# Performance work log

Measured on AMD Instinct MI355X. Metric: run time of the kernel, lower is better.

Reference implementation:

```python
import jax, jax.numpy as jnp
import numpy as np

# ---- DMP constants (from DMPParameters with N=5, tau=1, dt=1/(T*l), Dof=9, a_z=25) ----
N_BASIS = 5
T_STEPS = 10
L_SUB = 10
DIM = 9                      # len(state_index)
TAU = 1.0
DT = TAU / (T_STEPS * L_SUB)            # 0.01
TIME_STEPS = int(round(TAU / DT)) + 1   # 101
A_X = 1.0
A_Z = 25.0
B_Z = A_Z / 4.0
_c_np = np.exp(-A_X * np.linspace(0.0, 1.0, N_BASIS))
C = jnp.asarray(_c_np, dtype=jnp.float32)                          # rbf centers
H = jnp.asarray(N_BASIS ** 1.5 / _c_np / A_X, dtype=jnp.float32)   # rbf widths (sigma2)


def _integrate(w, y0, dy0, goal):
    """Euler integration of the DMP dynamical system.
    w: (R, N) basis weights; y0, dy0, goal: (R,) with R = batch*DIM.
    Returns Y: (R, TIME_STEPS) positions."""
    scale = goal - y0  # fixed forcing-term scaling

    def step(carry, _):
        y, z, x = carry
        x = x + (-A_X * x / TAU) * DT                  # canonical system
        psi = jnp.exp(-H * (x - C) ** 2)               # (N,) gaussian rbf
        fx = (w @ psi) * x * scale / jnp.sum(psi)      # (R,) forcing term
        dz = (A_Z * (B_Z * (goal - y) - z) + fx) / TAU
        dy = z / TAU
        y = y + dy * DT
        z = z + dz * DT
        return (y, z, x), y

    z0 = dy0 * TAU
    _, ys = jax.lax.scan(step, (y0, z0, jnp.float32(1.0)), None, length=TIME_STEPS - 1)
    # prepend initial position, transpose to (R, TIME_STEPS)
    return jnp.concatenate([y0[None, :], ys], axis=0).T


def setup_inputs():
    key = jax.random.key(0)
    ks = jax.random.split(key, 4)
    B, D_IN, HID = 16384, 128, 2048
    out_size = DIM * (N_BASIS + 1)  # 54 = N*dim + dim
    return {
        "input": jax.random.normal(ks[0], (B, D_IN), jnp.float32),
        "W0": jax.random.normal(ks[1], (HID, D_IN), jnp.float32) / np.sqrt(D_IN),
        "b0": jnp.full((HID,), 0.1, jnp.float32),
        "W1": jax.random.normal(ks[2], (HID, HID), jnp.float32) / np.sqrt(HID),
        "b1": jnp.full((HID,), 0.1, jnp.float32),
        "Wl": jax.random.normal(ks[3], (out_size, HID), jnp.float32) / np.sqrt(HID),
        "bl": jnp.zeros((out_size,), jnp.float32),
    }


def reference(input, W0, b0, W1, b1, Wl, bl):
    B = input.shape[0]
    # MLP backbone with tanh hidden activation
    h = jnp.tanh(input @ W0.T + b0)
    h = jnp.tanh(h @ W1.T + b1)
    out = (h @ Wl.T + bl) * 100.0                          # (B, DIM*(N+1))
    # split DMP parameters: goal then basis weights
    goal = out[:, :DIM].reshape(-1)                        # (B*DIM,)
    w = out[:, DIM:DIM * (N_BASIS + 1)].reshape(-1, N_BASIS)  # (B*DIM, N)
    y0 = input[:, 7:16].reshape(-1)                        # state_index
    dy0 = input[:, 22:31].reshape(-1)                      # vel_index
    Y = _integrate(w, y0, dy0, goal)                       # (B*DIM, 101)
    y = Y.reshape(B, DIM, TIME_STEPS)[:, :, ::L_SUB]       # (B, DIM, T+1)
    return y[:, :, 1:] - y[:, :, :-1]                      # (B, DIM, T)
```

## Files before the change

kernel.cpp:

```cpp
#include <hip/hip_runtime.h>
#include <hip/hip_fp16.h>
#include <math.h>

typedef _Float16 f16;
typedef _Float16 f16x8 __attribute__((ext_vector_type(8)));
typedef _Float16 f16x4v __attribute__((ext_vector_type(4)));
typedef float f32x4 __attribute__((ext_vector_type(4)));

#define B_SZ 16384
#define D_INP 128
#define HID 2048
#define DIMS 9
#define OUTC 54
#define OUTP 64
#define NZ3 4

__device__ __forceinline__ void load_lds16(const f16* g, f16* l) {
    __builtin_amdgcn_global_load_lds(
        (__attribute__((address_space(1))) void*)(g),
        (__attribute__((address_space(3))) void*)(l),
        16, 0, 0);
}

__device__ __forceinline__ float fast_tanh(float x) {
    float e = __builtin_amdgcn_exp2f(2.885390081777927f * x);
    return 1.0f - 2.0f * __builtin_amdgcn_rcpf(e + 1.0f);
}

#define N4_INP (B_SZ * D_INP / 4)
#define N4_W0  (HID * D_INP / 4)
#define N4_W1  (HID * HID / 4)
#define N4_WL  (OUTP * HID / 4)
__global__ __launch_bounds__(256) void cvt_fused_kernel(
    const float* __restrict__ input, const float* __restrict__ W0,
    const float* __restrict__ W1, const float* __restrict__ Wl,
    f16* __restrict__ inp16, f16* __restrict__ w0q,
    f16* __restrict__ w1q, f16* __restrict__ wlq)
{
    int i = blockIdx.x * 256 + threadIdx.x;
    const float* s; f16* d; int j;
    if (i < N4_INP) { s = input; d = inp16; j = i; }
    else if (i < N4_INP + N4_W0) { s = W0; d = w0q; j = i - N4_INP; }
    else if (i < N4_INP + N4_W0 + N4_W1) { s = W1; d = w1q; j = i - N4_INP - N4_W0; }
    else {
        j = i - N4_INP - N4_W0 - N4_W1;
        int e0 = j * 4, row = e0 >> 11, col = e0 & (HID - 1);
        f16x4v o;
        if (row < OUTC) {
            float4 v = ((const float4*)Wl)[(row * HID + col) >> 2];
            o.x = (f16)v.x; o.y = (f16)v.y; o.z = (f16)v.z; o.w = (f16)v.w;
        } else {
            o.x = (f16)0.f; o.y = (f16)0.f; o.z = (f16)0.f; o.w = (f16)0.f;
        }
        ((f16x4v*)wlq)[j] = o;
        return;
    }
    float4 v = ((const float4*)s)[j];
    f16x4v o;
    o.x = (f16)v.x; o.y = (f16)v.y; o.z = (f16)v.z; o.w = (f16)v.w;
    ((f16x4v*)d)[j] = o;
}

template <int BN, int EPI>
__global__ __launch_bounds__(256, 2) void gemm_nt(
    const f16* __restrict__ A, const f16* __restrict__ Bm,
    const float* __restrict__ bias, void* __restrict__ Cout,
    int M, int N, int K, int bias_n)
{
    constexpr int BM = 128, BK = 64;
    constexpr int NI = BN / 32;
    __shared__ __align__(16) f16 sa[BM * BK];
    __shared__ __align__(16) f16 sb[BN * BK];

    const int tid  = threadIdx.x;
    const int lane = tid & 63;
    const int wave = tid >> 6;
    const int wm = wave >> 1, wn = wave & 1;
    const int m0 = blockIdx.x * BM;
    const int n0 = blockIdx.y * BN;

    const int k_len = K / gridDim.z;
    const int k_beg = blockIdx.z * k_len;
    const int k_end = k_beg + k_len;

    f32x4 acc[4][NI];
    #pragma unroll
    for (int i = 0; i < 4; ++i)
        #pragma unroll
        for (int j = 0; j < NI; ++j) acc[i][j] = (f32x4){0.f, 0.f, 0.f, 0.f};

    const int r8 = lane >> 3;
    const int cg = (((lane & 7) ^ r8) << 3);

    for (int k0 = k_beg; k0 < k_end; k0 += BK) {
        #pragma unroll
        for (int c = 0; c < (BM * BK * 2) / 4096; ++c) {
            int o = c * 4096 + wave * 1024;
            const f16* gp = A + (size_t)(m0 + (o >> 7) + r8) * K + k0 + cg;
            load_lds16(gp, (f16*)((char*)sa + o));
        }
        #pragma unroll
        for (int c = 0; c < (BN * BK * 2) / 4096; ++c) {
            int o = c * 4096 + wave * 1024;
            const f16* gp = Bm + (size_t)(n0 + (o >> 7) + r8) * K + k0 + cg;
            load_lds16(gp, (f16*)((char*)sb + o));
        }
        __syncthreads();

        #pragma unroll
        for (int kc = 0; kc < 2; ++kc) {
            f16x8 af[4], bf[NI];
            #pragma unroll
            for (int mi = 0; mi < 4; ++mi) {
                int ar = wm * 64 + mi * 16 + (lane & 15);
                af[mi] = *(const f16x8*)&sa[ar * 64 + ((((kc << 2) | (lane >> 4)) ^ (ar & 7)) << 3)];
            }
            #pragma unroll
            for (int ni = 0; ni < NI; ++ni) {
                int br = wn * (BN / 2) + ni * 16 + (lane & 15);
                bf[ni] = *(const f16x8*)&sb[br * 64 + ((((kc << 2) | (lane >> 4)) ^ (br & 7)) << 3)];
            }
            #pragma unroll
            for (int mi = 0; mi < 4; ++mi)
                #pragma unroll
                for (int ni = 0; ni < NI; ++ni)
                    acc[mi][ni] = __builtin_amdgcn_mfma_f32_16x16x32_f16(af[mi], bf[ni], acc[mi][ni], 0, 0, 0);
        }
        __syncthreads();
    }

    const int crow0 = m0 + wm * 64 + (lane >> 4) * 4;
    const int ccol0 = n0 + wn * (BN / 2) + (lane & 15);
    if (EPI == 0) {
        f16* C = (f16*)Cout;
        #pragma unroll
        for (int mi = 0; mi < 4; ++mi)
            #pragma unroll
            for (int ni = 0; ni < NI; ++ni) {
                int col = ccol0 + ni * 16;
                float bv = bias[col];
                #pragma unroll
                for (int r2 = 0; r2 < 4; ++r2) {
                    float v = fast_tanh(acc[mi][ni][r2] + bv);
                    C[(size_t)(crow0 + mi * 16 + r2) * N + col] = (f16)v;
                }
            }
    } else {
        float* C = (float*)Cout + (size_t)blockIdx.z * M * N;
        #pragma unroll
        for (int mi = 0; mi < 4; ++mi)
            #pragma unroll
            for (int ni = 0; ni < NI; ++ni) {
                int col = ccol0 + ni * 16;
                float bv = (blockIdx.z == 0 && col < bias_n) ? bias[col] * 100.0f : 0.0f;
                #pragma unroll
                for (int r2 = 0; r2 < 4; ++r2) {
                    float v = acc[mi][ni][r2] * 100.0f + bv;
                    C[(size_t)(crow0 + mi * 16 + r2) * N + col] = v;
                }
            }
    }
}

__global__ __launch_bounds__(256) void integrate_kernel(
    const float* __restrict__ out3p, const float* __restrict__ input,
    float* __restrict__ out)
{
    __shared__ float g[500];
    {
        int k = threadIdx.x;
        if (k < 100) {
            float x = expf(-0.010050335853501441f * (float)(k + 1));
            float psi[5], ssum = 0.0f;
            #pragma unroll
            for (int n = 0; n < 5; ++n) {
                float c = expf(-0.25f * (float)n);
                float h = 11.180339887498949f / c;
                float dx = x - c;
                psi[n] = expf(-h * dx * dx);
                ssum += psi[n];
            }
            float inv = x / ssum;
            #pragma unroll
            for (int n = 0; n < 5; ++n) g[k * 5 + n] = psi[n] * inv;
        }
    }
    __syncthreads();

    int r = blockIdx.x * 256 + threadIdx.x;
    int b = r / DIMS, d = r - b * DIMS;

    float goal = 0.f, w0 = 0.f, w1 = 0.f, w2 = 0.f, w3 = 0.f, w4 = 0.f;
    #pragma unroll
    for (int z = 0; z < NZ3; ++z) {
        const float* ob = out3p + (size_t)z * B_SZ * OUTP + (size_t)b * OUTP;
        goal += ob[d];
        w0 += ob[DIMS + d * 5 + 0];
        w1 += ob[DIMS + d * 5 + 1];
        w2 += ob[DIMS + d * 5 + 2];
        w3 += ob[DIMS + d * 5 + 3];
        w4 += ob[DIMS + d * 5 + 4];
    }

    float y = input[(size_t)b * D_INP + 7 + d];
    float z = input[(size_t)b * D_INP + 22 + d];
    const float scale = goal - y;

    float prev = y;
    float* op = out + (size_t)b * (DIMS * 10) + d * 10;
    int j = 0;
    for (int k = 0; k < 100; ++k) {
        const float* gk = &g[k * 5];
        float fx = scale * (w0 * gk[0] + w1 * gk[1] + w2 * gk[2] + w3 * gk[3] + w4 * gk[4]);
        float dz = 25.0f * (6.25f * (goal - y) - z) + fx;
        y = y + z * 0.01f;
        z = z + dz * 0.01f;
        if ((k % 10) == 9) { op[j] = y - prev; prev = y; ++j; }
    }
}

extern "C" void kernel_launch(void* const* d_in, const int* in_sizes, int n_in,
                              void* d_out, int out_size, void* d_ws, size_t ws_size,
                              hipStream_t stream) {
    (void)in_sizes; (void)n_in; (void)out_size; (void)ws_size;
    const float* input = (const float*)d_in[0];
    const float* W0 = (const float*)d_in[1];
    const float* b0 = (const float*)d_in[2];
    const float* W1 = (const float*)d_in[3];
    const float* b1 = (const float*)d_in[4];
    const float* Wl = (const float*)d_in[5];
    const float* bl = (const float*)d_in[6];
    float* out = (float*)d_out;

    f16* inp16 = (f16*)d_ws;
    f16* w0q = inp16 + (size_t)B_SZ * D_INP;
    f16* w1q = w0q + (size_t)HID * D_INP;
    f16* wlq = w1q + (size_t)HID * HID;
    f16* h1  = wlq + (size_t)OUTP * HID;
    f16* h2  = h1 + (size_t)B_SZ * HID;
    float* out3p = (float*)h1;

    int n4_total = N4_INP + N4_W0 + N4_W1 + N4_WL;
    cvt_fused_kernel<<<(n4_total + 255) / 256, 256, 0, stream>>>(
        input, W0, W1, Wl, inp16, w0q, w1q, wlq);

    gemm_nt<128, 0><<<dim3(B_SZ / 128, HID / 128, 1), 256, 0, stream>>>(
        inp16, w0q, b0, (void*)h1, B_SZ, HID, D_INP, HID);
    gemm_nt<128, 0><<<dim3(B_SZ / 128, HID / 128, 1), 256, 0, stream>>>(
        h1, w1q, b1, (void*)h2, B_SZ, HID, HID, HID);
    gemm_nt<64, 1><<<dim3(B_SZ / 128, 1, NZ3), 256, 0, stream>>>(
        h2, wlq, bl, (void*)out3p, B_SZ, OUTP, HID, OUTC);

    integrate_kernel<<<B_SZ * DIMS / 256, 256, 0, stream>>>(out3p, input, out);
}
```

Before: 270.8 us.

## Switch GEMM to 32x32x16 MFMA tiles and add grouped block swizzle

Replaces the 16x16x32 MFMA micro-tiles with 32x32x16 MFMA, so each wave computes 2xNI 32x32 accumulators and the LDS fragment addressing and epilogue row mapping change to match. It also remaps block indices into groups of 8 M-tiles per N-column to improve L2 reuse of the B operand. The larger MFMA shape means fewer instructions and fewer LDS fragment loads per unit of compute. In exchange it needs larger accumulator vectors, and if BN is below 64 then NI becomes zero and the kernel computes nothing.

New measurement: 288.7 us. 1.07x slower.

```diff
diff --git a/kernel.cpp b/kernel.cpp
--- a/kernel.cpp
+++ b/kernel.cpp
@@ -5,7 +5,7 @@
 typedef _Float16 f16;
 typedef _Float16 f16x8 __attribute__((ext_vector_type(8)));
 typedef _Float16 f16x4v __attribute__((ext_vector_type(4)));
-typedef float f32x4 __attribute__((ext_vector_type(4)));
+typedef float f32x16 __attribute__((ext_vector_type(16)));
 
 #define B_SZ 16384
 #define D_INP 128
@@ -68,7 +68,7 @@
     int M, int N, int K, int bias_n)
 {
     constexpr int BM = 128, BK = 64;
-    constexpr int NI = BN / 32;
+    constexpr int NI = BN / 64;
     __shared__ __align__(16) f16 sa[BM * BK];
     __shared__ __align__(16) f16 sb[BN * BK];
 
@@ -76,18 +76,25 @@
     const int lane = tid & 63;
     const int wave = tid >> 6;
     const int wm = wave >> 1, wn = wave & 1;
-    const int m0 = blockIdx.x * BM;
-    const int n0 = blockIdx.y * BN;
+
+    const int flat = blockIdx.x + blockIdx.y * gridDim.x;
+    const int gsz  = 8 * gridDim.y;
+    const int grp  = flat / gsz;
+    const int rem  = flat - grp * gsz;
+    const int m0 = (grp * 8 + (rem & 7)) * BM;
+    const int n0 = (rem >> 3) * BN;
 
     const int k_len = K / gridDim.z;
     const int k_beg = blockIdx.z * k_len;
     const int k_end = k_beg + k_len;
 
-    f32x4 acc[4][NI];
+    f32x16 acc[2][NI];
     #pragma unroll
-    for (int i = 0; i < 4; ++i)
-        #pragma unroll
-        for (int j = 0; j < NI; ++j) acc[i][j] = (f32x4){0.f, 0.f, 0.f, 0.f};
+    for (int i = 0; i < 2; ++i)
+        #pragma unroll
+        for (int j = 0; j < NI; ++j)
+            #pragma unroll
+            for (int r = 0; r < 16; ++r) acc[i][j][r] = 0.f;
 
     const int r8 = lane >> 3;
     const int cg = (((lane & 7) ^ r8) << 3);
@@ -108,55 +115,58 @@
         __syncthreads();
 
         #pragma unroll
-        for (int kc = 0; kc < 2; ++kc) {
-            f16x8 af[4], bf[NI];
-            #pragma unroll
-            for (int mi = 0; mi < 4; ++mi) {
-                int ar = wm * 64 + mi * 16 + (lane & 15);
-                af[mi] = *(const f16x8*)&sa[ar * 64 + ((((kc << 2) | (lane >> 4)) ^ (ar & 7)) << 3)];
+        for (int kc = 0; kc < 4; ++kc) {
+            const int ch = kc * 2 + (lane >> 5);
+            f16x8 af[2], bf[NI];
+            #pragma unroll
+            for (int mi = 0; mi < 2; ++mi) {
+                int ar = wm * 64 + mi * 32 + (lane & 31);
+                af[mi] = *(const f16x8*)&sa[ar * 64 + ((ch ^ (ar & 7)) << 3)];
             }
             #pragma unroll
             for (int ni = 0; ni < NI; ++ni) {
-                int br = wn * (BN / 2) + ni * 16 + (lane & 15);
-                bf[ni] = *(const f16x8*)&sb[br * 64 + ((((kc << 2) | (lane >> 4)) ^ (br & 7)) << 3)];
-            }
-            #pragma unroll
-            for (int mi = 0; mi < 4; ++mi)
+                int br = wn * (BN / 2) + ni * 32 + (lane & 31);
+                bf[ni] = *(const f16x8*)&sb[br * 64 + ((ch ^ (br & 7)) << 3)];
+            }
+            #pragma unroll
+            for (int mi = 0; mi < 2; ++mi)
                 #pragma unroll
                 for (int ni = 0; ni < NI; ++ni)
-                    acc[mi][ni] = __builtin_amdgcn_mfma_f32_16x16x32_f16(af[mi], bf[ni], acc[mi][ni], 0, 0, 0);
+                    acc[mi][ni] = __builtin_amdgcn_mfma_f32_32x32x16_f16(af[mi], bf[ni], acc[mi][ni], 0, 0, 0);
         }
         __syncthreads();
     }
 
-    const int crow0 = m0 + wm * 64 + (lane >> 4) * 4;
-    const int ccol0 = n0 + wn * (BN / 2) + (lane & 15);
+    const int crow_b = m0 + wm * 64 + 4 * (lane >> 5);
+    const int ccol0 = n0 + wn * (BN / 2) + (lane & 31);
     if (EPI == 0) {
         f16* C = (f16*)Cout;
         #pragma unroll
-        for (int mi = 0; mi < 4; ++mi)
+        for (int mi = 0; mi < 2; ++mi)
             #pragma unroll
             for (int ni = 0; ni < NI; ++ni) {
-                int col = ccol0 + ni * 16;
+                int col = ccol0 + ni * 32;
                 float bv = bias[col];
                 #pragma unroll
-                for (int r2 = 0; r2 < 4; ++r2) {
-                    float v = fast_tanh(acc[mi][ni][r2] + bv);
-                    C[(size_t)(crow0 + mi * 16 + r2) * N + col] = (f16)v;
+                for (int r = 0; r < 16; ++r) {
+                    int row = crow_b + mi * 32 + (r & 3) + 8 * (r >> 2);
+                    float v = fast_tanh(acc[mi][ni][r] + bv);
+                    C[(size_t)row * N + col] = (f16)v;
                 }
             }
     } else {
         float* C = (float*)Cout + (size_t)blockIdx.z * M * N;
         #pragma unroll
-        for (int mi = 0; mi < 4; ++mi)
+        for (int mi = 0; mi < 2; ++mi)
             #pragma unroll
             for (int ni = 0; ni < NI; ++ni) {
-                int col = ccol0 + ni * 16;
+                int col = ccol0 + ni * 32;
                 float bv = (blockIdx.z == 0 && col < bias_n) ? bias[col] * 100.0f : 0.0f;
                 #pragma unroll
-                for (int r2 = 0; r2 < 4; ++r2) {
-                    float v = acc[mi][ni][r2] * 100.0f + bv;
-                    C[(size_t)(crow0 + mi * 16 + r2) * N + col] = v;
+                for (int r = 0; r < 16; ++r) {
+                    int row = crow_b + mi * 32 + (r & 3) + 8 * (r >> 2);
+                    float v = acc[mi][ni][r] * 100.0f + bv;
+                    C[(size_t)row * N + col] = v;
                 }
             }
     }
```

## Fuse input fp16 conversion into first GEMM and add grouped tile swizzle

Applied to the files above, without the earlier changes.

Removes the separate fp32→fp16 conversion of the input activations and instead loads fp32 input directly in a new first-layer GEMM kernel, converting to fp16 in registers before writing to LDS. This avoids a full write and read of the converted input buffer. The GEMM block index mapping is also changed to group eight M-tiles per column sweep, aiming to improve L2 reuse of the weight and activation tiles. The fp32 A loads go through registers rather than direct-to-LDS loads, which may add latency in the small-K first GEMM.

Result: faster. 256.8 us (-5.2%).

```diff
diff --git a/kernel.cpp b/kernel.cpp
--- a/kernel.cpp
+++ b/kernel.cpp
@@ -27,23 +27,20 @@
     return 1.0f - 2.0f * __builtin_amdgcn_rcpf(e + 1.0f);
 }
 
-#define N4_INP (B_SZ * D_INP / 4)
 #define N4_W0  (HID * D_INP / 4)
 #define N4_W1  (HID * HID / 4)
 #define N4_WL  (OUTP * HID / 4)
 __global__ __launch_bounds__(256) void cvt_fused_kernel(
-    const float* __restrict__ input, const float* __restrict__ W0,
-    const float* __restrict__ W1, const float* __restrict__ Wl,
-    f16* __restrict__ inp16, f16* __restrict__ w0q,
-    f16* __restrict__ w1q, f16* __restrict__ wlq)
+    const float* __restrict__ W0, const float* __restrict__ W1,
+    const float* __restrict__ Wl,
+    f16* __restrict__ w0q, f16* __restrict__ w1q, f16* __restrict__ wlq)
 {
     int i = blockIdx.x * 256 + threadIdx.x;
     const float* s; f16* d; int j;
-    if (i < N4_INP) { s = input; d = inp16; j = i; }
-    else if (i < N4_INP + N4_W0) { s = W0; d = w0q; j = i - N4_INP; }
-    else if (i < N4_INP + N4_W0 + N4_W1) { s = W1; d = w1q; j = i - N4_INP - N4_W0; }
+    if (i < N4_W0) { s = W0; d = w0q; j = i; }
+    else if (i < N4_W0 + N4_W1) { s = W1; d = w1q; j = i - N4_W0; }
     else {
-        j = i - N4_INP - N4_W0 - N4_W1;
+        j = i - N4_W0 - N4_W1;
         int e0 = j * 4, row = e0 >> 11, col = e0 & (HID - 1);
         f16x4v o;
         if (row < OUTC) {
@@ -76,8 +73,13 @@
     const int lane = tid & 63;
     const int wave = tid >> 6;
     const int wm = wave >> 1, wn = wave & 1;
-    const int m0 = blockIdx.x * BM;
-    const int n0 = blockIdx.y * BN;
+
+    const int flat = blockIdx.x + blockIdx.y * gridDim.x;
+    const int gsz  = 8 * gridDim.y;
+    const int grp  = flat / gsz;
+    const int rem  = flat - grp * gsz;
+    const int m0 = (grp * 8 + (rem & 7)) * BM;
+    const int n0 = (rem >> 3) * BN;
 
     const int k_len = K / gridDim.z;
     const int k_beg = blockIdx.z * k_len;
@@ -160,6 +162,94 @@
                 }
             }
     }
+}
+
+__global__ __launch_bounds__(256, 2) void gemm1_f32a(
+    const float* __restrict__ A, const f16* __restrict__ Bm,
+    const float* __restrict__ bias, f16* __restrict__ C)
+{
+    constexpr int BM = 128, BK = 64, BN = 128, NI = 4;
+    constexpr int N = HID, K = D_INP;
+    __shared__ __align__(16) f16 sa[BM * BK];
+    __shared__ __align__(16) f16 sb[BN * BK];
+
+    const int tid  = threadIdx.x;
+    const int lane = tid & 63;
+    const int wave = tid >> 6;
+    const int wm = wave >> 1, wn = wave & 1;
+
+    const int flat = blockIdx.x + blockIdx.y * gridDim.x;
+    const int gsz  = 8 * gridDim.y;
+    const int grp  = flat / gsz;
+    const int rem  = flat - grp * gsz;
+    const int m0 = (grp * 8 + (rem & 7)) * BM;
+    const int n0 = (rem >> 3) * BN;
+
+    f32x4 acc[4][NI];
+    #pragma unroll
+    for (int i = 0; i < 4; ++i)
+        #pragma unroll
+        for (int j = 0; j < NI; ++j) acc[i][j] = (f32x4){0.f, 0.f, 0.f, 0.f};
+
+    const int r8 = lane >> 3;
+    const int cg = (((lane & 7) ^ r8) << 3);
+
+    for (int k0 = 0; k0 < K; k0 += BK) {
+        #pragma unroll
+        for (int c = 0; c < (BM * BK * 2) / 4096; ++c) {
+            int o = c * 4096 + wave * 1024;
+            const float* gp = A + (size_t)(m0 + (o >> 7) + r8) * K + k0 + cg;
+            float4 v0 = *(const float4*)gp;
+            float4 v1 = *(const float4*)(gp + 4);
+            f16x8 h;
+            h[0] = (f16)v0.x; h[1] = (f16)v0.y; h[2] = (f16)v0.z; h[3] = (f16)v0.w;
+            h[4] = (f16)v1.x; h[5] = (f16)v1.y; h[6] = (f16)v1.z; h[7] = (f16)v1.w;
+            *(f16x8*)((char*)sa + o + (lane << 4)) = h;
+        }
+        #pragma unroll
+        for (int c = 0; c < (BN * BK * 2) / 4096; ++c) {
+            int o = c * 4096 + wave * 1024;
+            const f16* gp = Bm + (size_t)(n0 + (o >> 7) + r8) * K + k0 + cg;
+            load_lds16(gp, (f16*)((char*)sb + o));
+        }
+        __syncthreads();
+
+        #pragma unroll
+        for (int kc = 0; kc < 2; ++kc) {
+            f16x8 af[4], bf[NI];
+            #pragma unroll
+            for (int mi = 0; mi < 4; ++mi) {
+                int ar = wm * 64 + mi * 16 + (lane & 15);
+                af[mi] = *(const f16x8*)&sa[ar * 64 + ((((kc << 2) | (lane >> 4)) ^ (ar & 7)) << 3)];
+            }
+            #pragma unroll
+            for (int ni = 0; ni < NI; ++ni) {
+                int br = wn * 64 + ni * 16 + (lane & 15);
+                bf[ni] = *(const f16x8*)&sb[br * 64 + ((((kc << 2) | (lane >> 4)) ^ (br & 7)) << 3)];
+            }
+            #pragma unroll
+            for (int mi = 0; mi < 4; ++mi)
+                #pragma unroll
+                for (int ni = 0; ni < NI; ++ni)
+                    acc[mi][ni] = __builtin_amdgcn_mfma_f32_16x16x32_f16(af[mi], bf[ni], acc[mi][ni], 0, 0, 0);
+        }
+        __syncthreads();
+    }
+
+    const int crow0 = m0 + wm * 64 + (lane >> 4) * 4;
+    const int ccol0 = n0 + wn * 64 + (lane & 15);
+    #pragma unroll
+    for (int mi = 0; mi < 4; ++mi)
+        #pragma unroll
+        for (int ni = 0; ni < NI; ++ni) {
+            int col = ccol0 + ni * 16;
+            float bv = bias[col];
+            #pragma unroll
+            for (int r2 = 0; r2 < 4; ++r2) {
+                float v = fast_tanh(acc[mi][ni][r2] + bv);
+                C[(size_t)(crow0 + mi * 16 + r2) * N + col] = (f16)v;
+            }
+        }
 }
 
 __global__ __launch_bounds__(256) void integrate_kernel(
@@ -232,20 +322,19 @@
     const float* bl = (const float*)d_in[6];
     float* out = (float*)d_out;
 
-    f16* inp16 = (f16*)d_ws;
-    f16* w0q = inp16 + (size_t)B_SZ * D_INP;
+    f16* w0q = (f16*)d_ws;
     f16* w1q = w0q + (size_t)HID * D_INP;
     f16* wlq = w1q + (size_t)HID * HID;
     f16* h1  = wlq + (size_t)OUTP * HID;
     f16* h2  = h1 + (size_t)B_SZ * HID;
     float* out3p = (float*)h1;
 
-    int n4_total = N4_INP + N4_W0 + N4_W1 + N4_WL;
+    int n4_total = N4_W0 + N4_W1 + N4_WL;
     cvt_fused_kernel<<<(n4_total + 255) / 256, 256, 0, stream>>>(
-        input, W0, W1, Wl, inp16, w0q, w1q, wlq);
-
-    gemm_nt<128, 0><<<dim3(B_SZ / 128, HID / 128, 1), 256, 0, stream>>>(
-        inp16, w0q, b0, (void*)h1, B_SZ, HID, D_INP, HID);
+        W0, W1, Wl, w0q, w1q, wlq);
+
+    gemm1_f32a<<<dim3(B_SZ / 128, HID / 128), 256, 0, stream>>>(
+        input, w0q, b0, h1);
     gemm_nt<128, 0><<<dim3(B_SZ / 128, HID / 128, 1), 256, 0, stream>>>(
         h1, w1q, b1, (void*)h2, B_SZ, HID, HID, HID);
     gemm_nt<64, 1><<<dim3(B_SZ / 128, 1, NZ3), 256, 0, stream>>>(
```
